# Optimization experiments

Hardware: AMD Instinct MI355X
Metric: run time of the kernel (lower is better)

The kernel has to match this reference:

```python
import jax, jax.numpy as jnp
import numpy as np

# Sobel kernels stacked as 2 output channels of a 1-input-channel 3x3 conv: [2,1,3,3]
_SOBEL = jnp.array([
    [[[-1., 0., 1.], [-2., 0., 2.], [-1., 0., 1.]]],   # sobel_x
    [[[-1., -2., -1.], [0., 0., 0.], [1., 2., 1.]]],   # sobel_y
], dtype=jnp.float32)


def _edge_map(x):
    # x: [B, C, H, W] -> per-class edge magnitude |Gx| + |Gy|, same shape.
    B, C, H, W = x.shape
    xr = x.reshape(B * C, 1, H, W)  # fold classes into batch: one fused conv
    g = jax.lax.conv_general_dilated(
        xr, _SOBEL.astype(x.dtype),
        window_strides=(1, 1), padding=((1, 1), (1, 1)),
        dimension_numbers=("NCHW", "OIHW", "NCHW"))  # [B*C, 2, H, W]
    e = jnp.abs(g[:, 0]) + jnp.abs(g[:, 1])           # [B*C, H, W]
    return e.reshape(B, C, H, W)


def setup_inputs() -> dict:
    key = jax.random.key(0)
    k1, k2 = jax.random.split(key)
    B, C, H, W = 16, 19, 512, 512
    inputs = jax.random.normal(k1, (B, C, H, W), dtype=jnp.float32)
    targets = jax.random.randint(k2, (B, H, W), 0, C, dtype=jnp.int64)
    return {"inputs": inputs, "targets": targets}


def reference(inputs, targets):
    C = inputs.shape[1]
    targets_one_hot = jax.nn.one_hot(targets, C, axis=1, dtype=inputs.dtype)  # [B,C,H,W]
    edge_in = _edge_map(inputs)
    edge_tg = _edge_map(targets_one_hot)
    # F.mse_loss per class (mean over B,H,W) then summed over classes.
    sq = (edge_in - edge_tg) ** 2
    per_class = jnp.mean(sq, axis=(0, 2, 3))  # [C]
    return jnp.sum(per_class)
```

## Files before the change

kernel.cpp:

```cpp
#include <hip/hip_runtime.h>

namespace {
constexpr int B = 16, C = 19, H = 512, W = 512;
constexpr int BLOCK_W = 256;
constexpr int H_CHUNK = 128;
constexpr int NWB = W / BLOCK_W;
constexpr int NHC = H / H_CHUNK;
constexpr int TOTAL_BLOCKS = B * C * NWB * NHC;
constexpr float SCALE = 1.0f / (float)((long long)B * H * W);
}

__global__ void zero_out_kernel(float* out) { *out = 0.0f; }

__global__ __launch_bounds__(BLOCK_W) void edge_loss_kernel(
    const float* __restrict__ X,
    const int*   __restrict__ T,
    float* __restrict__ out)
{
    int bid = (int)blockIdx.x;
    const int c  = bid % C;   bid /= C;
    const int wb = bid % NWB; bid /= NWB;
    const int hc = bid % NHC; bid /= NHC;
    const int b  = bid;

    const int w  = wb * BLOCK_W + (int)threadIdx.x;
    const int h0 = hc * H_CHUNK;

    const float* __restrict__ Xs = X + (((size_t)b * C + c) * H) * (size_t)W;
    const int*   __restrict__ Ts = T + ((size_t)b * H) * (size_t)W;

    const bool wl = (w > 0), wr = (w < W - 1);
    const int wm = wl ? (w - 1) : 0;
    const int wp = wr ? (w + 1) : (W - 1);
    const float fl = wl ? 1.0f : 0.0f;
    const float fr = wr ? 1.0f : 0.0f;

    float x00,x01,x02, x10,x11,x12, x20,x21,x22;
    float m00,m01,m02, m10,m11,m12, m20,m21,m22;

    const float* xrow = Xs + (size_t)h0 * W;
    const int*   trow = Ts + (size_t)h0 * W;

    if (h0 > 0) {
        const float* xp = xrow - W;
        const int*   tp = trow - W;
        x00 = xp[wm] * fl; x01 = xp[w]; x02 = xp[wp] * fr;
        const int t0 = tp[wm], t1 = tp[w], t2 = tp[wp];
        m00 = (t0 == c) ? fl : 0.0f;
        m01 = (t1 == c) ? 1.0f : 0.0f;
        m02 = (t2 == c) ? fr : 0.0f;
    } else {
        x00 = x01 = x02 = 0.0f; m00 = m01 = m02 = 0.0f;
    }
    {
        x10 = xrow[wm] * fl; x11 = xrow[w]; x12 = xrow[wp] * fr;
        const int t0 = trow[wm], t1 = trow[w], t2 = trow[wp];
        m10 = (t0 == c) ? fl : 0.0f;
        m11 = (t1 == c) ? 1.0f : 0.0f;
        m12 = (t2 == c) ? fr : 0.0f;
    }

    const float* xn = xrow + W;
    const int*   tn = trow + W;

    float acc = 0.0f;
    #pragma unroll 4
    for (int h = h0; h < h0 + H_CHUNK; ++h) {
        if (h + 1 < H) {
            x20 = xn[wm] * fl; x21 = xn[w]; x22 = xn[wp] * fr;
            const int t0 = tn[wm], t1 = tn[w], t2 = tn[wp];
            m20 = (t0 == c) ? fl : 0.0f;
            m21 = (t1 == c) ? 1.0f : 0.0f;
            m22 = (t2 == c) ? fr : 0.0f;
        } else {
            x20 = x21 = x22 = 0.0f; m20 = m21 = m22 = 0.0f;
        }
        xn += W; tn += W;

        float gx = (x02 - x00) + 2.0f*(x12 - x10) + (x22 - x20);
        float gy = (x20 + 2.0f*x21 + x22) - (x00 + 2.0f*x01 + x02);
        float ein = fabsf(gx) + fabsf(gy);

        float hx = (m02 - m00) + 2.0f*(m12 - m10) + (m22 - m20);
        float hy = (m20 + 2.0f*m21 + m22) - (m00 + 2.0f*m01 + m02);
        float etg = fabsf(hx) + fabsf(hy);

        const float d = ein - etg;
        acc = fmaf(d, d, acc);

        x00 = x10; x01 = x11; x02 = x12;
        x10 = x20; x11 = x21; x12 = x22;
        m00 = m10; m01 = m11; m02 = m12;
        m10 = m20; m11 = m21; m12 = m22;
    }

    #pragma unroll
    for (int off = 32; off > 0; off >>= 1)
        acc += __shfl_down(acc, off, 64);

    __shared__ float wsum[BLOCK_W / 64];
    const int lane = (int)threadIdx.x & 63;
    const int wid  = (int)threadIdx.x >> 6;
    if (lane == 0) wsum[wid] = acc;
    __syncthreads();
    if (threadIdx.x == 0) {
        const float s = wsum[0] + wsum[1] + wsum[2] + wsum[3];
        atomicAdd(out, s * SCALE);
    }
}

extern "C" void kernel_launch(void* const* d_in, const int* in_sizes, int n_in,
                              void* d_out, int out_size, void* d_ws, size_t ws_size,
                              hipStream_t stream) {
    (void)in_sizes; (void)n_in; (void)d_ws; (void)ws_size; (void)out_size;
    const float* X = (const float*)d_in[0];
    const int*   T = (const int*)d_in[1];
    float* out = (float*)d_out;

    zero_out_kernel<<<1, 1, 0, stream>>>(out);
    edge_loss_kernel<<<TOTAL_BLOCKS, BLOCK_W, 0, stream>>>(X, T, out);
}
```

Measured before the change: 112.1 us.

## Vectorize Sobel loss with float4 rows, wave shuffles, separable sums and XCD-aware tiling

Each thread now handles four adjacent columns, loading one float4 of inputs and one int4 of targets per row. Horizontal neighbours come from wave shuffles instead of redundant scalar loads. Per-row horizontal differences and smoothed sums are precomputed and rotated through a three-row register ring, making the Sobel separable. Blocks are remapped so the 19 class blocks sharing a batch/row tile land on the same XCD and can reuse the target rows in L2. Costs include more registers per thread and an extra edge-column load for the boundary lanes.

```diff
diff --git a/kernel.cpp b/kernel.cpp
--- a/kernel.cpp
+++ b/kernel.cpp
@@ -2,111 +2,129 @@
 
 namespace {
 constexpr int B = 16, C = 19, H = 512, W = 512;
-constexpr int BLOCK_W = 256;
-constexpr int H_CHUNK = 128;
-constexpr int NWB = W / BLOCK_W;
+constexpr int TPB = 128;
+constexpr int H_CHUNK = 64;
 constexpr int NHC = H / H_CHUNK;
-constexpr int TOTAL_BLOCKS = B * C * NWB * NHC;
+constexpr int TILES = B * NHC;
+constexpr int NXCD = 8;
+constexpr int TILES_PER_XCD = TILES / NXCD;
+constexpr int TOTAL_BLOCKS = TILES * C;
 constexpr float SCALE = 1.0f / (float)((long long)B * H * W);
 }
 
+struct RowS {
+    float4 d, s;
+    float4 md, ms;
+};
+
 __global__ void zero_out_kernel(float* out) { *out = 0.0f; }
 
-__global__ __launch_bounds__(BLOCK_W) void edge_loss_kernel(
+__global__ __launch_bounds__(TPB) void edge_loss_kernel(
     const float* __restrict__ X,
     const int*   __restrict__ T,
     float* __restrict__ out)
 {
-    int bid = (int)blockIdx.x;
-    const int c  = bid % C;   bid /= C;
-    const int wb = bid % NWB; bid /= NWB;
-    const int hc = bid % NHC; bid /= NHC;
-    const int b  = bid;
+    int i = (int)blockIdx.x;
+    const int xcd = i & (NXCD - 1);
+    const int j   = i >> 3;
+    const int c   = j % C;
+    const int tl  = j / C;
+    const int tile = xcd * TILES_PER_XCD + tl;
+    const int b   = tile / NHC;
+    const int hc  = tile % NHC;
 
-    const int w  = wb * BLOCK_W + (int)threadIdx.x;
-    const int h0 = hc * H_CHUNK;
+    const int tid  = (int)threadIdx.x;
+    const int lane = tid & 63;
+    const int w0   = tid << 2;
+    const int h0   = hc * H_CHUNK;
 
-    const float* __restrict__ Xs = X + (((size_t)b * C + c) * H) * (size_t)W;
-    const int*   __restrict__ Ts = T + ((size_t)b * H) * (size_t)W;
+    const float* __restrict__ Xs = X + (size_t)(b * C + c) * (size_t)(H * W);
+    const int*   __restrict__ Ts = T + (size_t)b * (size_t)(H * W);
 
-    const bool wl = (w > 0), wr = (w < W - 1);
-    const int wm = wl ? (w - 1) : 0;
-    const int wp = wr ? (w + 1) : (W - 1);
-    const float fl = wl ? 1.0f : 0.0f;
-    const float fr = wr ? 1.0f : 0.0f;
+    const bool needL = (lane == 0)  && (w0 > 0);
+    const bool needR = (lane == 63) && (w0 + 4 < W);
+    const int  colL  = needL ? (w0 - 1) : 0;
+    const int  colR  = needR ? (w0 + 4) : 0;
 
-    float x00,x01,x02, x10,x11,x12, x20,x21,x22;
-    float m00,m01,m02, m10,m11,m12, m20,m21,m22;
+    RowS r0, r1, r2;
+    float acc = 0.0f;
 
-    const float* xrow = Xs + (size_t)h0 * W;
-    const int*   trow = Ts + (size_t)h0 * W;
+    auto load_row = [&](RowS& r, int hrow) {
+        if (hrow < 0 || hrow >= H) {
+            r.d = r.s = r.md = r.ms = make_float4(0.f, 0.f, 0.f, 0.f);
+            return;
+        }
+        const float* xr = Xs + (size_t)hrow * W;
+        const int*   tr = Ts + (size_t)hrow * W;
+        const float4 xv = *reinterpret_cast<const float4*>(xr + w0);
+        const int4   tv = *reinterpret_cast<const int4*>(tr + w0);
+        const float eL  = needL ? xr[colL] : 0.0f;
+        const float eR  = needR ? xr[colR] : 0.0f;
+        const float eLm = needL ? ((tr[colL] == c) ? 1.0f : 0.0f) : 0.0f;
+        const float eRm = needR ? ((tr[colR] == c) ? 1.0f : 0.0f) : 0.0f;
 
-    if (h0 > 0) {
-        const float* xp = xrow - W;
-        const int*   tp = trow - W;
-        x00 = xp[wm] * fl; x01 = xp[w]; x02 = xp[wp] * fr;
-        const int t0 = tp[wm], t1 = tp[w], t2 = tp[wp];
-        m00 = (t0 == c) ? fl : 0.0f;
-        m01 = (t1 == c) ? 1.0f : 0.0f;
-        m02 = (t2 == c) ? fr : 0.0f;
-    } else {
-        x00 = x01 = x02 = 0.0f; m00 = m01 = m02 = 0.0f;
+        float Lx = __shfl_up(xv.w, 1, 64);   if (lane == 0)  Lx = eL;
+        float Rx = __shfl_down(xv.x, 1, 64); if (lane == 63) Rx = eR;
+
+        const float m0 = (tv.x == c) ? 1.0f : 0.0f;
+        const float m1 = (tv.y == c) ? 1.0f : 0.0f;
+        const float m2 = (tv.z == c) ? 1.0f : 0.0f;
+        const float m3 = (tv.w == c) ? 1.0f : 0.0f;
+        float Lm = __shfl_up(m3, 1, 64);     if (lane == 0)  Lm = eLm;
+        float Rm = __shfl_down(m0, 1, 64);   if (lane == 63) Rm = eRm;
+
+        r.d.x = xv.y - Lx;   r.d.y = xv.z - xv.x;
+        r.d.z = xv.w - xv.y; r.d.w = Rx   - xv.z;
+        r.s.x = fmaf(2.f, xv.x, Lx + xv.y);
+        r.s.y = fmaf(2.f, xv.y, xv.x + xv.z);
+        r.s.z = fmaf(2.f, xv.z, xv.y + xv.w);
+        r.s.w = fmaf(2.f, xv.w, xv.z + Rx);
+
+        r.md.x = m1 - Lm; r.md.y = m2 - m0;
+        r.md.z = m3 - m1; r.md.w = Rm - m2;
+        r.ms.x = fmaf(2.f, m0, Lm + m1);
+        r.ms.y = fmaf(2.f, m1, m0 + m2);
+        r.ms.z = fmaf(2.f, m2, m1 + m3);
+        r.ms.w = fmaf(2.f, m3, m2 + Rm);
+    };
+
+    int h = h0;
+    auto body = [&](const RowS& ra, const RowS& rb, RowS& rc) {
+        load_row(rc, h + 1);
+#define COMP(f)                                                      \
+        {                                                            \
+            float gx = fmaf(2.f, rb.d.f,  ra.d.f  + rc.d.f);         \
+            float gy = rc.s.f  - ra.s.f;                             \
+            float hx = fmaf(2.f, rb.md.f, ra.md.f + rc.md.f);        \
+            float hy = rc.ms.f - ra.ms.f;                            \
+            float dd = (fabsf(gx) + fabsf(gy))                       \
+                     - (fabsf(hx) + fabsf(hy));                      \
+            acc = fmaf(dd, dd, acc);                                 \
+        }
+        COMP(x) COMP(y) COMP(z) COMP(w)
+#undef COMP
+        ++h;
+    };
+
+    load_row(r0, h0 - 1);
+    load_row(r1, h0);
+
+    for (int t = 0; t < (H_CHUNK / 3); ++t) {
+        body(r0, r1, r2);
+        body(r1, r2, r0);
+        body(r2, r0, r1);
     }
-    {
-        x10 = xrow[wm] * fl; x11 = xrow[w]; x12 = xrow[wp] * fr;
-        const int t0 = trow[wm], t1 = trow[w], t2 = trow[wp];
-        m10 = (t0 == c) ? fl : 0.0f;
-        m11 = (t1 == c) ? 1.0f : 0.0f;
-        m12 = (t2 == c) ? fr : 0.0f;
-    }
-
-    const float* xn = xrow + W;
-    const int*   tn = trow + W;
-
-    float acc = 0.0f;
-    #pragma unroll 4
-    for (int h = h0; h < h0 + H_CHUNK; ++h) {
-        if (h + 1 < H) {
-            x20 = xn[wm] * fl; x21 = xn[w]; x22 = xn[wp] * fr;
-            const int t0 = tn[wm], t1 = tn[w], t2 = tn[wp];
-            m20 = (t0 == c) ? fl : 0.0f;
-            m21 = (t1 == c) ? 1.0f : 0.0f;
-            m22 = (t2 == c) ? fr : 0.0f;
-        } else {
-            x20 = x21 = x22 = 0.0f; m20 = m21 = m22 = 0.0f;
-        }
-        xn += W; tn += W;
-
-        float gx = (x02 - x00) + 2.0f*(x12 - x10) + (x22 - x20);
-        float gy = (x20 + 2.0f*x21 + x22) - (x00 + 2.0f*x01 + x02);
-        float ein = fabsf(gx) + fabsf(gy);
-
-        float hx = (m02 - m00) + 2.0f*(m12 - m10) + (m22 - m20);
-        float hy = (m20 + 2.0f*m21 + m22) - (m00 + 2.0f*m01 + m02);
-        float etg = fabsf(hx) + fabsf(hy);
-
-        const float d = ein - etg;
-        acc = fmaf(d, d, acc);
-
-        x00 = x10; x01 = x11; x02 = x12;
-        x10 = x20; x11 = x21; x12 = x22;
-        m00 = m10; m01 = m11; m02 = m12;
-        m10 = m20; m11 = m21; m12 = m22;
-    }
+    body(r0, r1, r2);
 
     #pragma unroll
     for (int off = 32; off > 0; off >>= 1)
         acc += __shfl_down(acc, off, 64);
 
-    __shared__ float wsum[BLOCK_W / 64];
-    const int lane = (int)threadIdx.x & 63;
-    const int wid  = (int)threadIdx.x >> 6;
+    __shared__ float wsum[TPB / 64];
+    const int wid = tid >> 6;
     if (lane == 0) wsum[wid] = acc;
     __syncthreads();
-    if (threadIdx.x == 0) {
-        const float s = wsum[0] + wsum[1] + wsum[2] + wsum[3];
-        atomicAdd(out, s * SCALE);
-    }
+    if (tid == 0) atomicAdd(out, (wsum[0] + wsum[1]) * SCALE);
 }
 
 extern "C" void kernel_launch(void* const* d_in, const int* in_sizes, int n_in,
@@ -118,5 +136,5 @@
     float* out = (float*)d_out;
 
     zero_out_kernel<<<1, 1, 0, stream>>>(out);
-    edge_loss_kernel<<<TOTAL_BLOCKS, BLOCK_W, 0, stream>>>(X, T, out);
+    edge_loss_kernel<<<TOTAL_BLOCKS, TPB, 0, stream>>>(X, T, out);
 }
```

New measurement: 139.5 us. +24.4%, slower.
